# Kernel optimization log

Hardware: AMD Instinct MI355X
Metric: run time of the kernel (lower is better)

## Reference

```python
import jax, jax.numpy as jnp
import numpy as np

HEADS = 16

def setup_inputs() -> dict:
    key = jax.random.key(0)
    k1, k2, k3 = jax.random.split(key, 3)
    T, B, E = 2048, 4, 1024
    query = jax.random.normal(k1, (T, B, E), dtype=jnp.float32)
    in_proj_weight = jax.random.normal(k2, (3 * E, E), dtype=jnp.float32) * (E ** -0.5)
    out_proj_weight = jax.random.normal(k3, (E, E), dtype=jnp.float32) * (E ** -0.5)
    return {"query": query, "in_proj_weight": in_proj_weight, "out_proj_weight": out_proj_weight}

def reference(query, in_proj_weight, out_proj_weight):
    # query: [T, B, E] (time-first, as in apex SelfMultiheadAttn)
    T, B, E = query.shape
    H = HEADS
    D = E // H
    scale = D ** -0.5
    # fused in-projection: x @ W_in^T -> [T, B, 3E]
    qkv = jnp.einsum('tbe,fe->tbf', query, in_proj_weight)
    q, k, v = jnp.split(qkv, 3, axis=-1)
    # [T, B, E] -> [B, H, T, D]
    def to_bhtd(x):
        return x.reshape(T, B, H, D).transpose(1, 2, 0, 3)
    q = to_bhtd(q) * scale
    k = to_bhtd(k)
    v = to_bhtd(v)
    scores = jnp.einsum('bhqd,bhkd->bhqk', q, k)  # [B, H, T, T]
    # causal (mask_future_timesteps=True) time mask
    causal = jnp.tril(jnp.ones((T, T), dtype=bool))
    scores = jnp.where(causal, scores, jnp.finfo(scores.dtype).min)
    attn = jax.nn.softmax(scores, axis=-1)
    # dropout_prob = 0.0 -> identity
    ctx = jnp.einsum('bhqk,bhkd->bhqd', attn, v)  # [B, H, T, D]
    ctx = ctx.transpose(2, 0, 1, 3).reshape(T, B, E)
    out = jnp.einsum('tbe,fe->tbf', ctx, out_proj_weight)
    return out
```

## Files before the change

kernel.cpp:

```cpp
#include <hip/hip_runtime.h>


typedef float  f32x4  __attribute__((ext_vector_type(4)));
typedef short  s16x8  __attribute__((ext_vector_type(8)));
typedef __bf16 bf16x8 __attribute__((ext_vector_type(8)));

#define T_DIM 2048
#define B_DIM 4
#define E_DIM 1024
#define PLANE (T_DIM * 64)

__device__ inline unsigned short f2bf(float f) {
  return (unsigned short)((__builtin_bit_cast(unsigned int, f) + 0x8000u) >> 16);
}

__device__ inline f32x4 mfma16(s16x8 a, s16x8 b, f32x4 c) {
  return __builtin_amdgcn_mfma_f32_16x16x32_bf16(
      __builtin_bit_cast(bf16x8, a), __builtin_bit_cast(bf16x8, b), c, 0, 0, 0);
}

__device__ inline void gl2lds16(const unsigned short* g, unsigned short* l) {
  __builtin_amdgcn_global_load_lds(
      (__attribute__((address_space(1))) unsigned int*)g,
      (__attribute__((address_space(3))) unsigned int*)l, 16, 0, 0);
}

__device__ inline unsigned packbf(float a, float b) {
  return __builtin_amdgcn_perm(__builtin_bit_cast(unsigned, b),
                               __builtin_bit_cast(unsigned, a), 0x07060302u);
}

__global__ __launch_bounds__(256)
void cvt_bf16(const float* __restrict__ in, unsigned short* __restrict__ out,
              int n4) {
  int i = blockIdx.x * 256 + threadIdx.x;
  if (i >= n4) return;
  float4 v = ((const float4*)in)[i];
  ushort4 o;
  o.x = f2bf(v.x); o.y = f2bf(v.y); o.z = f2bf(v.z); o.w = f2bf(v.w);
  ((ushort4*)out)[i] = o;
}

__global__ __launch_bounds__(256)
void cvt_bf16_scaled(const float* __restrict__ in,
                     unsigned short* __restrict__ out, int n4, float scale) {
  int i = blockIdx.x * 256 + threadIdx.x;
  if (i >= n4) return;
  float4 v = ((const float4*)in)[i];
  ushort4 o;
  o.x = f2bf(v.x * scale); o.y = f2bf(v.y * scale);
  o.z = f2bf(v.z * scale); o.w = f2bf(v.w * scale);
  ((ushort4*)out)[i] = o;
}

__global__ __launch_bounds__(256, 2)
void gemm256(const unsigned short* __restrict__ A,
             const unsigned short* __restrict__ Bw,
             unsigned short* __restrict__ Cq, int K) {
  __shared__ __attribute__((aligned(16))) unsigned short As[256 * 64];
  __shared__ __attribute__((aligned(16))) unsigned short Bs[128 * 64];

  const int tid = threadIdx.x, lane = tid & 63, w = tid >> 6;
  const int row16 = lane & 15, quad = lane >> 4;
  const int m0 = blockIdx.y * 256, n0 = blockIdx.x * 128;
  const int wm = (w & 1) * 128, wn = (w >> 1) * 64;
  const int srow = lane >> 3;
  const int jsw = (lane & 7) ^ srow;
  const int sw7 = row16 & 7;

  f32x4 acc[8][4];
  for (int i = 0; i < 8; ++i)
    for (int j = 0; j < 4; ++j) acc[i][j] = (f32x4){0.f, 0.f, 0.f, 0.f};

  for (int k0 = 0; k0 < K; k0 += 64) {
    for (int i2 = 0; i2 < 8; ++i2) {
      int ia = w * 8 + i2;
      int r = ia * 8 + srow;
      gl2lds16(A + (size_t)(m0 + r) * K + k0 + jsw * 8, &As[ia * 512]);
    }
    for (int i2 = 0; i2 < 4; ++i2) {
      int ib = w * 4 + i2;
      int r = ib * 8 + srow;
      gl2lds16(Bw + (size_t)(n0 + r) * K + k0 + jsw * 8, &Bs[ib * 512]);
    }
    __syncthreads();
    for (int kk = 0; kk < 2; ++kk) {
      s16x8 af[8], bfr[4];
      for (int mi = 0; mi < 8; ++mi)
        af[mi] = *(const s16x8*)&As[(wm + mi * 16 + row16) * 64 +
                                    (((kk * 4 + quad) ^ sw7) * 8)];
      for (int ni = 0; ni < 4; ++ni)
        bfr[ni] = *(const s16x8*)&Bs[(wn + ni * 16 + row16) * 64 +
                                     (((kk * 4 + quad) ^ sw7) * 8)];
      for (int mi = 0; mi < 8; ++mi)
        for (int ni = 0; ni < 4; ++ni)
          acc[mi][ni] = mfma16(af[mi], bfr[ni], acc[mi][ni]);
    }
    __syncthreads();
  }

  if (n0 >= 2048) {
    const int hw = ((n0 & 1023) >> 6) + (w >> 1);
    const int tg0 = (m0 >> 2) + (w & 1) * 32;
    unsigned short* tb = &As[w * 2560];
    for (int bb = 0; bb < 4; ++bb) {
      for (int mi = 0; mi < 8; ++mi)
        for (int ni = 0; ni < 4; ++ni)
          tb[(ni * 16 + row16) * 40 + mi * 4 + quad] = f2bf(acc[mi][ni][bb]);
      asm volatile("s_waitcnt lgkmcnt(0)" ::: "memory");
      unsigned short* vp = Cq + (size_t)(128 + bb * 16 + hw) * PLANE;
      for (int it = 0; it < 4; ++it) {
        int dd = it * 16 + (lane >> 2);
        int tl = (lane & 3) * 8;
        s16x8 v = *(const s16x8*)&tb[dd * 40 + tl];
        *(s16x8*)(vp + (size_t)dd * T_DIM + tg0 + tl) = v;
      }
      asm volatile("s_waitcnt lgkmcnt(0)" ::: "memory");
    }
  } else {
    for (int mi = 0; mi < 8; ++mi)
      for (int ni = 0; ni < 4; ++ni)
        for (int r = 0; r < 4; ++r) {
          int m = m0 + wm + mi * 16 + quad * 4 + r;
          int n = n0 + wn + ni * 16 + row16;
          int t = m >> 2, bb = m & 3;
          int which = n >> 10, hh = (n >> 6) & 15, dd = n & 63;
          Cq[(size_t)(which * 64 + bb * 16 + hh) * PLANE + (size_t)t * 64 + dd] =
              f2bf(acc[mi][ni][r]);
        }
  }
}

__global__ __launch_bounds__(256)
void gemm128(const unsigned short* __restrict__ A,
             const unsigned short* __restrict__ Bw,
             float* __restrict__ Cf, int N, int K) {
  __shared__ __attribute__((aligned(16))) unsigned short As[128 * 64];
  __shared__ __attribute__((aligned(16))) unsigned short Bs[128 * 64];

  const int tid = threadIdx.x, lane = tid & 63, w = tid >> 6;
  const int row16 = lane & 15, quad = lane >> 4;
  const int m0 = blockIdx.y * 128, n0 = blockIdx.x * 128;
  const int wm = (w & 1) * 64, wn = (w >> 1) * 64;
  const int srow = lane >> 3;
  const int jsw = (lane & 7) ^ srow;
  const int sw7 = row16 & 7;

  f32x4 acc[4][4];
  for (int i = 0; i < 4; ++i)
    for (int j = 0; j < 4; ++j) acc[i][j] = (f32x4){0.f, 0.f, 0.f, 0.f};

  for (int k0 = 0; k0 < K; k0 += 64) {
    for (int i = 0; i < 4; ++i) {
      int ia = i * 4 + w;
      int r = ia * 8 + srow;
      gl2lds16(A  + (size_t)(m0 + r) * K + k0 + jsw * 8, &As[ia * 512]);
      gl2lds16(Bw + (size_t)(n0 + r) * K + k0 + jsw * 8, &Bs[ia * 512]);
    }
    __syncthreads();
    for (int kk = 0; kk < 2; ++kk) {
      s16x8 af[4], bfr[4];
      for (int mi = 0; mi < 4; ++mi)
        af[mi] = *(const s16x8*)&As[(wm + mi * 16 + row16) * 64 +
                                    (((kk * 4 + quad) ^ sw7) * 8)];
      for (int ni = 0; ni < 4; ++ni)
        bfr[ni] = *(const s16x8*)&Bs[(wn + ni * 16 + row16) * 64 +
                                     (((kk * 4 + quad) ^ sw7) * 8)];
      for (int mi = 0; mi < 4; ++mi)
        for (int ni = 0; ni < 4; ++ni)
          acc[mi][ni] = mfma16(af[mi], bfr[ni], acc[mi][ni]);
    }
    __syncthreads();
  }

  for (int mi = 0; mi < 4; ++mi)
    for (int ni = 0; ni < 4; ++ni)
      for (int r = 0; r < 4; ++r) {
        int m = m0 + wm + mi * 16 + quad * 4 + r;
        int n = n0 + wn + ni * 16 + row16;
        Cf[(size_t)m * N + n] = acc[mi][ni][r];
      }
}

__global__ __launch_bounds__(256)
void attn_fwd(const unsigned short* __restrict__ qkv,
              unsigned short* __restrict__ ctx) {
  __shared__ __attribute__((aligned(16))) unsigned short Ks[2][4096];
  __shared__ __attribute__((aligned(16))) unsigned short Vs[2][4096];
  __shared__ __attribute__((aligned(16))) unsigned short Ps[4][2048];

  const int tid = threadIdx.x, lane = tid & 63, w = tid >> 6;
  const int row16 = lane & 15, quad = lane >> 4;
  const int bh = blockIdx.x >> 4;
  const int qt = 15 - (blockIdx.x & 15);
  const int b = bh >> 4, h = bh & 15;

  const unsigned short* Qg = qkv + (size_t)bh * PLANE;
  const unsigned short* Kg = qkv + (size_t)(64 + bh) * PLANE;
  const unsigned short* Vt = qkv + (size_t)(128 + bh) * PLANE;

  const int r8 = lane >> 3;
  const int jsw = (lane & 7) ^ r8;
  const int sw7 = row16 & 7;

  auto stage = [&](int c, int buf) {
    for (int i2 = 0; i2 < 2; ++i2) {
      int i = w + i2 * 4;
      int r = i * 8 + r8;
      gl2lds16(Kg + (size_t)(c * 64 + r) * 64 + jsw * 8, &Ks[buf][i * 512]);
      gl2lds16(Vt + (size_t)r * T_DIM + c * 64 + jsw * 8, &Vs[buf][i * 512]);
    }
  };

  const int q0w = qt * 128 + w * 32;
  const int cmax = 2 * qt + 1;
  const int dc = 2 * qt + (w >> 1);

  s16x8 qb[2][2];
  for (int nq = 0; nq < 2; ++nq)
    for (int s = 0; s < 2; ++s)
      qb[nq][s] = *(const s16x8*)(Qg + (size_t)(q0w + nq * 16 + row16) * 64 +
                                  s * 32 + quad * 8);

  f32x4 O[4][2];
  for (int md = 0; md < 4; ++md)
    for (int nq = 0; nq < 2; ++nq) O[md][nq] = (f32x4){0.f, 0.f, 0.f, 0.f};
  float lp[2] = {0.f, 0.f};

  stage(0, 0);
  __syncthreads();

  for (int c = 0; c <= cmax; ++c) {
    const int buf = c & 1;
    if (c < cmax) stage(c + 1, buf ^ 1);

    if (c <= dc) {
      f32x4 S[4][2];
      for (int nt = 0; nt < 4; ++nt)
        for (int nq = 0; nq < 2; ++nq) S[nt][nq] = (f32x4){0.f, 0.f, 0.f, 0.f};
      for (int nt = 0; nt < 4; ++nt)
        for (int s = 0; s < 2; ++s) {
          s16x8 ka = *(const s16x8*)&Ks[buf][(nt * 16 + row16) * 64 +
                                            (((s * 4 + quad) ^ sw7) * 8)];
          for (int nq = 0; nq < 2; ++nq)
            S[nt][nq] = mfma16(ka, qb[nq][s], S[nt][nq]);
        }

      auto softmax_store = [&](bool diagm) {
        for (int nq = 0; nq < 2; ++nq) {
          const int qg = q0w + nq * 16 + row16;
          for (int nt = 0; nt < 4; ++nt) {
            float pv[4];
            for (int r = 0; r < 4; ++r) {
              pv[r] = __builtin_amdgcn_exp2f(S[nt][nq][r]);
              if (diagm && (c * 64 + nt * 16 + quad * 4 + r) > qg) pv[r] = 0.f;
              lp[nq] += pv[r];
            }
            int qr = nq * 16 + row16;
            int pos = (nt * 2 + (quad >> 1)) ^ sw7;
            *(uint2*)&Ps[w][qr * 64 + pos * 8 + (quad & 1) * 4] =
                make_uint2(packbf(pv[0], pv[1]), packbf(pv[2], pv[3]));
          }
        }
      };
      if (c == dc) softmax_store(true); else softmax_store(false);
      asm volatile("s_waitcnt lgkmcnt(0)" ::: "memory");

      for (int sk = 0; sk < 2; ++sk) {
        s16x8 pb[2];
        for (int nq = 0; nq < 2; ++nq)
          pb[nq] = *(const s16x8*)&Ps[w][(nq * 16 + row16) * 64 +
                                         (((sk * 4 + quad) ^ sw7) * 8)];
        for (int md = 0; md < 4; ++md) {
          s16x8 va = *(const s16x8*)&Vs[buf][(md * 16 + row16) * 64 +
                                            (((sk * 4 + quad) ^ sw7) * 8)];
          for (int nq = 0; nq < 2; ++nq)
            O[md][nq] = mfma16(va, pb[nq], O[md][nq]);
        }
      }
    }
    __syncthreads();
  }

  for (int nq = 0; nq < 2; ++nq) {
    float s = lp[nq];
    s += __shfl_xor(s, 16);
    s += __shfl_xor(s, 32);
    float inv = 1.f / s;
    const int t = q0w + nq * 16 + row16;
    for (int md = 0; md < 4; ++md) {
      unsigned lo = packbf(O[md][nq][0] * inv, O[md][nq][1] * inv);
      unsigned hi = packbf(O[md][nq][2] * inv, O[md][nq][3] * inv);
      *(uint2*)&ctx[((size_t)t * B_DIM + b) * E_DIM + h * 64 + md * 16 +
                    quad * 4] = make_uint2(lo, hi);
    }
  }
}

extern "C" void kernel_launch(void* const* d_in, const int* in_sizes, int n_in,
                              void* d_out, int out_size, void* d_ws,
                              size_t ws_size, hipStream_t stream) {
  const float* query = (const float*)d_in[0];
  const float* win   = (const float*)d_in[1];
  const float* wout  = (const float*)d_in[2];
  float* out = (float*)d_out;

  unsigned short* qkvb = (unsigned short*)d_ws;
  unsigned short* ctxb = qkvb + (size_t)3 * B_DIM * 16 * T_DIM * 64;
  unsigned short* xb   = ctxb;
  unsigned short* winb = (unsigned short*)d_out;
  unsigned short* woutb = qkvb;

  const float QSCALE = 0.18033688011112042f;

  cvt_bf16<<<8192, 256, 0, stream>>>(query, xb, (8192 * 1024) / 4);
  cvt_bf16_scaled<<<1024, 256, 0, stream>>>(win, winb, (1024 * 1024) / 4,
                                            QSCALE);
  cvt_bf16<<<2048, 256, 0, stream>>>(win + 1024 * 1024, winb + 1024 * 1024,
                                     (2048 * 1024) / 4);
  gemm256<<<dim3(3072 / 128, 8192 / 256), 256, 0, stream>>>(xb, winb, qkvb,
                                                            1024);
  attn_fwd<<<dim3(1024), 256, 0, stream>>>(qkvb, ctxb);
  cvt_bf16<<<1024, 256, 0, stream>>>(wout, woutb, (1024 * 1024) / 4);
  gemm128<<<dim3(8, 64), 256, 0, stream>>>(ctxb, woutb, out, 1024, 1024);
}
```

Measured before the change: 278.7 us.

## Pair causal query tiles per block and deepen attention K/V pipeline to four stages

The attention kernel now launches 512 blocks, and each block handles two query tiles (p and 15-p), so per-block causal work is roughly equal. The K/V staging ring grows from two to four buffers with three chunks prefetched ahead, and a vmcnt wait plus barrier replaces the trailing __syncthreads. MFMA sections are raised with s_setprio. The two weight-conversion launches are merged into one kernel that picks its scale by index. The larger LDS footprint may lower occupancy, and the hand-counted vmcnt waits depend on how many loads each stage issues.

```diff
diff --git a/kernel.cpp b/kernel.cpp
--- a/kernel.cpp
+++ b/kernel.cpp
@@ -42,14 +42,14 @@
 }
 
 __global__ __launch_bounds__(256)
-void cvt_bf16_scaled(const float* __restrict__ in,
-                     unsigned short* __restrict__ out, int n4, float scale) {
+void cvt_w_in(const float* __restrict__ in, unsigned short* __restrict__ out,
+              float qs) {
   int i = blockIdx.x * 256 + threadIdx.x;
-  if (i >= n4) return;
+  float sc = (i < (E_DIM * E_DIM / 4)) ? qs : 1.0f;
   float4 v = ((const float4*)in)[i];
   ushort4 o;
-  o.x = f2bf(v.x * scale); o.y = f2bf(v.y * scale);
-  o.z = f2bf(v.z * scale); o.w = f2bf(v.w * scale);
+  o.x = f2bf(v.x * sc); o.y = f2bf(v.y * sc);
+  o.z = f2bf(v.z * sc); o.w = f2bf(v.w * sc);
   ((ushort4*)out)[i] = o;
 }
 
@@ -185,14 +185,14 @@
 __global__ __launch_bounds__(256)
 void attn_fwd(const unsigned short* __restrict__ qkv,
               unsigned short* __restrict__ ctx) {
-  __shared__ __attribute__((aligned(16))) unsigned short Ks[2][4096];
-  __shared__ __attribute__((aligned(16))) unsigned short Vs[2][4096];
+  __shared__ __attribute__((aligned(16))) unsigned short Ks[4][4096];
+  __shared__ __attribute__((aligned(16))) unsigned short Vs[4][4096];
   __shared__ __attribute__((aligned(16))) unsigned short Ps[4][2048];
 
   const int tid = threadIdx.x, lane = tid & 63, w = tid >> 6;
   const int row16 = lane & 15, quad = lane >> 4;
-  const int bh = blockIdx.x >> 4;
-  const int qt = 15 - (blockIdx.x & 15);
+  const int bh = blockIdx.x;
+  const int p  = blockIdx.y;
   const int b = bh >> 4, h = bh & 15;
 
   const unsigned short* Qg = qkv + (size_t)bh * PLANE;
@@ -212,87 +212,100 @@
     }
   };
 
-  const int q0w = qt * 128 + w * 32;
-  const int cmax = 2 * qt + 1;
-  const int dc = 2 * qt + (w >> 1);
-
-  s16x8 qb[2][2];
-  for (int nq = 0; nq < 2; ++nq)
-    for (int s = 0; s < 2; ++s)
-      qb[nq][s] = *(const s16x8*)(Qg + (size_t)(q0w + nq * 16 + row16) * 64 +
-                                  s * 32 + quad * 8);
-
-  f32x4 O[4][2];
-  for (int md = 0; md < 4; ++md)
-    for (int nq = 0; nq < 2; ++nq) O[md][nq] = (f32x4){0.f, 0.f, 0.f, 0.f};
-  float lp[2] = {0.f, 0.f};
-
-  stage(0, 0);
-  __syncthreads();
-
-  for (int c = 0; c <= cmax; ++c) {
-    const int buf = c & 1;
-    if (c < cmax) stage(c + 1, buf ^ 1);
-
-    if (c <= dc) {
-      f32x4 S[4][2];
-      for (int nt = 0; nt < 4; ++nt)
-        for (int nq = 0; nq < 2; ++nq) S[nt][nq] = (f32x4){0.f, 0.f, 0.f, 0.f};
-      for (int nt = 0; nt < 4; ++nt)
-        for (int s = 0; s < 2; ++s) {
-          s16x8 ka = *(const s16x8*)&Ks[buf][(nt * 16 + row16) * 64 +
-                                            (((s * 4 + quad) ^ sw7) * 8)];
+  for (int half = 0; half < 2; ++half) {
+    const int qt = half ? p : (15 - p);
+    const int q0w = qt * 128 + w * 32;
+    const int cmax = 2 * qt + 1;
+    const int dc = 2 * qt + (w >> 1);
+
+    s16x8 qb[2][2];
+    for (int nq = 0; nq < 2; ++nq)
+      for (int s = 0; s < 2; ++s)
+        qb[nq][s] = *(const s16x8*)(Qg + (size_t)(q0w + nq * 16 + row16) * 64 +
+                                    s * 32 + quad * 8);
+
+    f32x4 O[4][2];
+    for (int md = 0; md < 4; ++md)
+      for (int nq = 0; nq < 2; ++nq) O[md][nq] = (f32x4){0.f, 0.f, 0.f, 0.f};
+    float lp[2] = {0.f, 0.f};
+
+    if (half) __builtin_amdgcn_s_barrier();
+    stage(0, 0);
+    stage(1, 1);
+    if (cmax >= 2) stage(2, 2);
+
+    for (int c = 0; c <= cmax; ++c) {
+      const int buf = c & 3;
+      const int rem = cmax - c;
+      if (rem >= 2)      asm volatile("s_waitcnt vmcnt(8)" ::: "memory");
+      else if (rem == 1) asm volatile("s_waitcnt vmcnt(4)" ::: "memory");
+      else               asm volatile("s_waitcnt vmcnt(0)" ::: "memory");
+      __builtin_amdgcn_s_barrier();
+      if (c + 3 <= cmax) stage(c + 3, (c + 3) & 3);
+
+      if (c <= dc) {
+        f32x4 S[4][2];
+        for (int nt = 0; nt < 4; ++nt)
+          for (int nq = 0; nq < 2; ++nq) S[nt][nq] = (f32x4){0.f, 0.f, 0.f, 0.f};
+        __builtin_amdgcn_s_setprio(1);
+        for (int nt = 0; nt < 4; ++nt)
+          for (int s = 0; s < 2; ++s) {
+            s16x8 ka = *(const s16x8*)&Ks[buf][(nt * 16 + row16) * 64 +
+                                              (((s * 4 + quad) ^ sw7) * 8)];
+            for (int nq = 0; nq < 2; ++nq)
+              S[nt][nq] = mfma16(ka, qb[nq][s], S[nt][nq]);
+          }
+        __builtin_amdgcn_s_setprio(0);
+
+        auto softmax_store = [&](bool diagm) {
+          for (int nq = 0; nq < 2; ++nq) {
+            const int qg = q0w + nq * 16 + row16;
+            for (int nt = 0; nt < 4; ++nt) {
+              float pv[4];
+              for (int r = 0; r < 4; ++r) {
+                pv[r] = __builtin_amdgcn_exp2f(S[nt][nq][r]);
+                if (diagm && (c * 64 + nt * 16 + quad * 4 + r) > qg) pv[r] = 0.f;
+                lp[nq] += pv[r];
+              }
+              int qr = nq * 16 + row16;
+              int pos = (nt * 2 + (quad >> 1)) ^ sw7;
+              *(uint2*)&Ps[w][qr * 64 + pos * 8 + (quad & 1) * 4] =
+                  make_uint2(packbf(pv[0], pv[1]), packbf(pv[2], pv[3]));
+            }
+          }
+        };
+        if (c == dc) softmax_store(true); else softmax_store(false);
+        asm volatile("s_waitcnt lgkmcnt(0)" ::: "memory");
+
+        __builtin_amdgcn_s_setprio(1);
+        for (int sk = 0; sk < 2; ++sk) {
+          s16x8 pb[2];
           for (int nq = 0; nq < 2; ++nq)
-            S[nt][nq] = mfma16(ka, qb[nq][s], S[nt][nq]);
-        }
-
-      auto softmax_store = [&](bool diagm) {
-        for (int nq = 0; nq < 2; ++nq) {
-          const int qg = q0w + nq * 16 + row16;
-          for (int nt = 0; nt < 4; ++nt) {
-            float pv[4];
-            for (int r = 0; r < 4; ++r) {
-              pv[r] = __builtin_amdgcn_exp2f(S[nt][nq][r]);
-              if (diagm && (c * 64 + nt * 16 + quad * 4 + r) > qg) pv[r] = 0.f;
-              lp[nq] += pv[r];
-            }
-            int qr = nq * 16 + row16;
-            int pos = (nt * 2 + (quad >> 1)) ^ sw7;
-            *(uint2*)&Ps[w][qr * 64 + pos * 8 + (quad & 1) * 4] =
-                make_uint2(packbf(pv[0], pv[1]), packbf(pv[2], pv[3]));
+            pb[nq] = *(const s16x8*)&Ps[w][(nq * 16 + row16) * 64 +
+                                           (((sk * 4 + quad) ^ sw7) * 8)];
+          for (int md = 0; md < 4; ++md) {
+            s16x8 va = *(const s16x8*)&Vs[buf][(md * 16 + row16) * 64 +
+                                              (((sk * 4 + quad) ^ sw7) * 8)];
+            for (int nq = 0; nq < 2; ++nq)
+              O[md][nq] = mfma16(va, pb[nq], O[md][nq]);
           }
         }
-      };
-      if (c == dc) softmax_store(true); else softmax_store(false);
-      asm volatile("s_waitcnt lgkmcnt(0)" ::: "memory");
-
-      for (int sk = 0; sk < 2; ++sk) {
-        s16x8 pb[2];
-        for (int nq = 0; nq < 2; ++nq)
-          pb[nq] = *(const s16x8*)&Ps[w][(nq * 16 + row16) * 64 +
-                                         (((sk * 4 + quad) ^ sw7) * 8)];
-        for (int md = 0; md < 4; ++md) {
-          s16x8 va = *(const s16x8*)&Vs[buf][(md * 16 + row16) * 64 +
-                                            (((sk * 4 + quad) ^ sw7) * 8)];
-          for (int nq = 0; nq < 2; ++nq)
-            O[md][nq] = mfma16(va, pb[nq], O[md][nq]);
-        }
+        __builtin_amdgcn_s_setprio(0);
       }
     }
-    __syncthreads();
-  }
-
-  for (int nq = 0; nq < 2; ++nq) {
-    float s = lp[nq];
-    s += __shfl_xor(s, 16);
-    s += __shfl_xor(s, 32);
-    float inv = 1.f / s;
-    const int t = q0w + nq * 16 + row16;
-    for (int md = 0; md < 4; ++md) {
-      unsigned lo = packbf(O[md][nq][0] * inv, O[md][nq][1] * inv);
-      unsigned hi = packbf(O[md][nq][2] * inv, O[md][nq][3] * inv);
-      *(uint2*)&ctx[((size_t)t * B_DIM + b) * E_DIM + h * 64 + md * 16 +
-                    quad * 4] = make_uint2(lo, hi);
+
+    for (int nq = 0; nq < 2; ++nq) {
+      float s = lp[nq];
+      s += __shfl_xor(s, 16);
+      s += __shfl_xor(s, 32);
+      float inv = 1.f / s;
+      const int t = q0w + nq * 16 + row16;
+      for (int md = 0; md < 4; ++md) {
+        unsigned lo = packbf(O[md][nq][0] * inv, O[md][nq][1] * inv);
+        unsigned hi = packbf(O[md][nq][2] * inv, O[md][nq][3] * inv);
+        *(uint2*)&ctx[((size_t)t * B_DIM + b) * E_DIM + h * 64 + md * 16 +
+                      quad * 4] = make_uint2(lo, hi);
+      }
     }
   }
 }
@@ -314,13 +327,10 @@
   const float QSCALE = 0.18033688011112042f;
 
   cvt_bf16<<<8192, 256, 0, stream>>>(query, xb, (8192 * 1024) / 4);
-  cvt_bf16_scaled<<<1024, 256, 0, stream>>>(win, winb, (1024 * 1024) / 4,
-                                            QSCALE);
-  cvt_bf16<<<2048, 256, 0, stream>>>(win + 1024 * 1024, winb + 1024 * 1024,
-                                     (2048 * 1024) / 4);
+  cvt_w_in<<<3072, 256, 0, stream>>>(win, winb, QSCALE);
   gemm256<<<dim3(3072 / 128, 8192 / 256), 256, 0, stream>>>(xb, winb, qkvb,
                                                             1024);
-  attn_fwd<<<dim3(1024), 256, 0, stream>>>(qkvb, ctxb);
+  attn_fwd<<<dim3(64, 8), 256, 0, stream>>>(qkvb, ctxb);
   cvt_bf16<<<1024, 256, 0, stream>>>(wout, woutb, (1024 * 1024) / 4);
   gemm128<<<dim3(8, 64), 256, 0, stream>>>(ctxb, woutb, out, 1024, 1024);
 }
```

Result: faster. 243.8 us (-12.5%).
